# Performance work log

Hardware: AMD Instinct MI355X
Metric: run time of the kernel (lower is better)

Reference implementation:

```python
import jax, jax.numpy as jnp
import numpy as np

B, H, DH = 1, 16, 128
HID, MLP = 2048, 8192
LT, LI = 256, 2048
L = LT + LI


def _layernorm(x, eps=1e-6):
    mu = jnp.mean(x, axis=-1, keepdims=True)
    var = jnp.mean((x - mu) ** 2, axis=-1, keepdims=True)
    return (x - mu) * jax.lax.rsqrt(var + eps)


def _rmsnorm(x, scale, eps=1e-6):
    rr = jax.lax.rsqrt(jnp.mean(x * x, axis=-1, keepdims=True) + eps)
    return x * rr * scale


def _apply_rope(x, pe):
    # x: (B,H,L,D) -> (B,H,L,D/2,1,2); pe: (B,1,L,D/2,2,2)
    xs = x.reshape(*x.shape[:-1], -1, 1, 2)
    out = pe[..., 0] * xs[..., 0] + pe[..., 1] * xs[..., 1]  # (B,H,L,D/2,2)
    return out.reshape(x.shape)


def _qkv_split(x, w, b):
    Bv, Lv, _ = x.shape
    qkv = (x @ w + b).reshape(Bv, Lv, 3, H, DH).transpose(2, 0, 3, 1, 4)  # K B H L D
    return qkv[0], qkv[1], qkv[2]


def setup_inputs() -> dict:
    key = jax.random.key(0)
    ks = jax.random.split(key, 16)
    s = 0.02
    inp = {
        'img': jax.random.normal(ks[0], (B, LI, HID), jnp.float32),
        'txt': jax.random.normal(ks[1], (B, LT, HID), jnp.float32),
        'vec': jax.random.normal(ks[2], (B, HID), jnp.float32),
        'img_mod_w': s * jax.random.normal(ks[3], (HID, 6 * HID), jnp.float32),
        'img_mod_b': jnp.zeros((6 * HID,), jnp.float32),
        'txt_mod_w': s * jax.random.normal(ks[4], (HID, 6 * HID), jnp.float32),
        'txt_mod_b': jnp.zeros((6 * HID,), jnp.float32),
        'img_qkv_w': s * jax.random.normal(ks[5], (HID, 3 * HID), jnp.float32),
        'img_qkv_b': jnp.zeros((3 * HID,), jnp.float32),
        'img_q_scale': jnp.ones((DH,), jnp.float32),
        'img_k_scale': jnp.ones((DH,), jnp.float32),
        'txt_qkv_w': s * jax.random.normal(ks[6], (HID, 3 * HID), jnp.float32),
        'txt_qkv_b': jnp.zeros((3 * HID,), jnp.float32),
        'txt_q_scale': jnp.ones((DH,), jnp.float32),
        'txt_k_scale': jnp.ones((DH,), jnp.float32),
        'img_proj_w': s * jax.random.normal(ks[7], (HID, HID), jnp.float32),
        'img_proj_b': jnp.zeros((HID,), jnp.float32),
        'txt_proj_w': s * jax.random.normal(ks[8], (HID, HID), jnp.float32),
        'txt_proj_b': jnp.zeros((HID,), jnp.float32),
        'img_mlp_w1': s * jax.random.normal(ks[9], (HID, MLP), jnp.float32),
        'img_mlp_b1': jnp.zeros((MLP,), jnp.float32),
        'img_mlp_w2': s * jax.random.normal(ks[10], (MLP, HID), jnp.float32),
        'img_mlp_b2': jnp.zeros((HID,), jnp.float32),
        'txt_mlp_w1': s * jax.random.normal(ks[11], (HID, MLP), jnp.float32),
        'txt_mlp_b1': jnp.zeros((MLP,), jnp.float32),
        'txt_mlp_w2': s * jax.random.normal(ks[12], (MLP, HID), jnp.float32),
        'txt_mlp_b2': jnp.zeros((HID,), jnp.float32),
    }
    # Real RoPE rotation matrices [[cos,-sin],[sin,cos]]: (1,1,L,DH/2,2,2)
    pos = jnp.arange(L, dtype=jnp.float32)
    freqs = 1.0 / (10000.0 ** (jnp.arange(DH // 2, dtype=jnp.float32) / (DH // 2)))
    ang = pos[:, None] * freqs[None, :]
    c, sn = jnp.cos(ang), jnp.sin(ang)
    pe = jnp.stack([jnp.stack([c, -sn], -1), jnp.stack([sn, c], -1)], -2)  # (L,DH/2,2,2)
    inp['pe'] = pe[None, None]
    return inp


def reference(img, txt, vec, pe,
              img_mod_w, img_mod_b, txt_mod_w, txt_mod_b,
              img_qkv_w, img_qkv_b, img_q_scale, img_k_scale,
              txt_qkv_w, txt_qkv_b, txt_q_scale, txt_k_scale,
              img_proj_w, img_proj_b, txt_proj_w, txt_proj_b,
              img_mlp_w1, img_mlp_b1, img_mlp_w2, img_mlp_b2,
              txt_mlp_w1, txt_mlp_b1, txt_mlp_w2, txt_mlp_b2):
    # AdaLN modulation: SiLU(vec) @ W -> 6 chunks of (B,1,HID)
    im = jnp.split(jax.nn.silu(vec) @ img_mod_w + img_mod_b, 6, axis=-1)
    i_sh1, i_sc1, i_g1, i_sh2, i_sc2, i_g2 = [m[:, None, :] for m in im]
    tm = jnp.split(jax.nn.silu(vec) @ txt_mod_w + txt_mod_b, 6, axis=-1)
    t_sh1, t_sc1, t_g1, t_sh2, t_sc2, t_g2 = [m[:, None, :] for m in tm]

    img_mod = (1 + i_sc1) * _layernorm(img) + i_sh1
    iq, ik, iv = _qkv_split(img_mod, img_qkv_w, img_qkv_b)
    iq = _rmsnorm(iq, img_q_scale)
    ik = _rmsnorm(ik, img_k_scale)

    txt_mod = (1 + t_sc1) * _layernorm(txt) + t_sh1
    tq, tk, tv = _qkv_split(txt_mod, txt_qkv_w, txt_qkv_b)
    tq = _rmsnorm(tq, txt_q_scale)
    tk = _rmsnorm(tk, txt_k_scale)

    # concat text then image along sequence (B,H,L,D)
    q = jnp.concatenate([tq, iq], axis=2)
    k = jnp.concatenate([tk, ik], axis=2)
    v = jnp.concatenate([tv, iv], axis=2)
    q = _apply_rope(q, pe)
    k = _apply_rope(k, pe)

    scores = jnp.einsum('bhqd,bhkd->bhqk', q, k) / np.float32(np.sqrt(DH))
    a = jax.nn.softmax(scores, axis=-1)
    o = jnp.einsum('bhqk,bhkd->bhqd', a, v)
    attn = o.transpose(0, 2, 1, 3).reshape(o.shape[0], -1, H * DH)  # (B,L,HID)

    txt_a, img_a = attn[:, :LT], attn[:, LT:]

    img = img + i_g1 * (img_a @ img_proj_w + img_proj_b)
    h = (1 + i_sc2) * _layernorm(img) + i_sh2
    h = jax.nn.gelu(h @ img_mlp_w1 + img_mlp_b1, approximate=True)
    img = img + i_g2 * (h @ img_mlp_w2 + img_mlp_b2)

    txt = txt + t_g1 * (txt_a @ txt_proj_w + txt_proj_b)
    h = (1 + t_sc2) * _layernorm(txt) + t_sh2
    h = jax.nn.gelu(h @ txt_mlp_w1 + txt_mlp_b1, approximate=True)
    txt = txt + t_g2 * (h @ txt_mlp_w2 + txt_mlp_b2)

    return img, txt
```

## Files before the change

kernel.cpp:

```cpp
#include <hip/hip_runtime.h>

using u16 = unsigned short;
typedef __bf16 bf16x8 __attribute__((ext_vector_type(8)));
typedef float f32x4 __attribute__((ext_vector_type(4)));

__device__ inline u16 f2bf(float f){
  unsigned u = __float_as_uint(f);
  u += 0x7fff + ((u >> 16) & 1);
  return (u16)(u >> 16);
}
__device__ inline float bf2f(u16 u){ return __uint_as_float((unsigned)u << 16); }

__device__ inline float wredsum(float v){
  #pragma unroll
  for (int o = 32; o; o >>= 1) v += __shfl_xor(v, o, 64);
  return v;
}
__device__ inline float wredmax(float v){
  #pragma unroll
  for (int o = 32; o; o >>= 1) v = fmaxf(v, __shfl_xor(v, o, 64));
  return v;
}

__device__ inline void gld16(const u16* g, u16* lds){
  __builtin_amdgcn_global_load_lds(
      (const __attribute__((address_space(1))) unsigned int*)g,
      (__attribute__((address_space(3))) unsigned int*)lds, 16, 0, 0);
}

__global__ void mod_matvec_k(const float* __restrict__ vec,
    const float* __restrict__ wi, const float* __restrict__ bi,
    const float* __restrict__ wt, const float* __restrict__ bt,
    float* __restrict__ oi, float* __restrict__ ot)
{
  __shared__ float sv[2048];
  __shared__ float red[4][64];
  int tid = threadIdx.x;
  for (int i = tid; i < 2048; i += 256){ float v = vec[i]; sv[i] = v / (1.0f + __expf(-v)); }
  __syncthreads();
  int j0 = blockIdx.x * 64;
  bool ist = j0 >= 12288;
  const float* w = ist ? wt : wi;
  const float* b = ist ? bt : bi;
  float* o = ist ? ot : oi;
  int col = (ist ? j0 - 12288 : j0) + (tid & 63);
  int kq = tid >> 6;
  float acc = 0.f;
  const float* wp = w + col;
  for (int k = kq * 512; k < kq * 512 + 512; ++k) acc += sv[k] * wp[(long long)k * 12288];
  red[kq][tid & 63] = acc;
  __syncthreads();
  if (kq == 0){
    o[col] = red[0][tid] + red[1][tid] + red[2][tid] + red[3][tid] + b[col];
  }
}

struct TcArgs {
  const float* in[8];
  u16* out[8];
  int K[8];
  int N[8];
  int base[9];
};

__global__ void tcast8_k(TcArgs a)
{
  __shared__ float tile[32][33];
  int bid = blockIdx.x;
  int w = 0;
  #pragma unroll
  for (int i = 0; i < 8; ++i) if (bid >= a.base[i + 1]) w = i + 1;
  const float* in = a.in[w];
  u16* out = a.out[w];
// ... 44 lines not shown

__global__ void qkv_post_k(const float* __restrict__ qkv, int pos0,
    const float* __restrict__ qs, const float* __restrict__ ks,
    const float* __restrict__ pe,
    u16* __restrict__ Q, u16* __restrict__ Ko, u16* __restrict__ Vt)
{
  __shared__ u16 vs[128][72];
  int h = blockIdx.y;
  int t0 = blockIdx.x * 64;
  int tid = threadIdx.x, wave = tid >> 6, lane = tid & 63;
  for (int it = 0; it < 16; ++it){
    int tl = it * 4 + wave;
    int t = t0 + tl;
    const float* rp = qkv + (long long)t * 6144 + h * 128;
    float q0 = rp[lane],        q1 = rp[lane + 64];
    float k0 = rp[2048 + lane], k1 = rp[2048 + lane + 64];
    float v0 = rp[4096 + lane], v1 = rp[4096 + lane + 64];
    float qss = wredsum(q0 * q0 + q1 * q1);
    float kss = wredsum(k0 * k0 + k1 * k1);
    float rq = rsqrtf(qss * (1.0f / 128.0f) + 1e-6f) * 0.08838834764831845f;
    float rk = rsqrtf(kss * (1.0f / 128.0f) + 1e-6f);
    float qn0 = q0 * rq * qs[lane], qn1 = q1 * rq * qs[lane + 64];
    float kn0 = k0 * rk * ks[lane], kn1 = k1 * rk * ks[lane + 64];
    int pos = pos0 + t;
    const float* peb = pe + (long long)pos * 256;
    bool odd = lane & 1;
    float4 p0 = *(const float4*)&peb[(lane >> 1) * 4];
    float4 p1 = *(const float4*)&peb[128 + (lane >> 1) * 4];
    float c00 = odd ? p0.z : p0.x, c01 = odd ? p0.w : p0.y;
    float c10 = odd ? p1.z : p1.x, c11 = odd ? p1.w : p1.y;
    float qp0 = __shfl_xor(qn0, 1, 64), qp1 = __shfl_xor(qn1, 1, 64);
    float kp0 = __shfl_xor(kn0, 1, 64), kp1 = __shfl_xor(kn1, 1, 64);
    float qe0 = odd ? qp0 : qn0, qo0 = odd ? qn0 : qp0;
    float qe1 = odd ? qp1 : qn1, qo1 = odd ? qn1 : qp1;
    float ke0 = odd ? kp0 : kn0, ko0 = odd ? kn0 : kp0;
    float ke1 = odd ? kp1 : kn1, ko1 = odd ? kn1 : kp1;
    u16* Qr = Q  + ((long long)h * 2304 + pos) * 128;
    u16* Kr = Ko + ((long long)h * 2304 + pos) * 128;
    Qr[lane]      = f2bf(c00 * qe0 + c01 * qo0);
    Qr[lane + 64] = f2bf(c10 * qe1 + c11 * qo1);
    Kr[lane]      = f2bf(c00 * ke0 + c01 * ko0);
    Kr[lane + 64] = f2bf(c10 * ke1 + c11 * ko1);
    vs[lane][tl]      = f2bf(v0);
    vs[lane + 64][tl] = f2bf(v1);
  }
  __syncthreads();
  int dd = tid >> 1, co = (tid & 1) * 32;
  u16* vr = Vt + ((long long)h * 128 + dd) * 2304 + pos0 + t0 + co;
  #pragma unroll
  for (int u = 0; u < 8; ++u)
    *(ushort4*)(vr + u * 4) = *(const ushort4*)&vs[dd][co + u * 4];
}

__global__ void softmax16_k(u16* __restrict__ S)
{
  long long base = (long long)blockIdx.y * 2304 * 2304 + (long long)blockIdx.x * 2304;
  u16* row = S + base;
  int tid = threadIdx.x;
  float v[9]; float m = -3.0e38f;
  #pragma unroll
  for (int j = 0; j < 9; ++j){ v[j] = bf2f(row[tid + j * 256]); m = fmaxf(m, v[j]); }
  m = wredmax(m);
  __shared__ float red[4];
  int wave = tid >> 6, lane = tid & 63;
  if (lane == 0) red[wave] = m;
  __syncthreads();
  m = fmaxf(fmaxf(red[0], red[1]), fmaxf(red[2], red[3]));
  float s = 0.f;
  #pragma unroll
  for (int j = 0; j < 9; ++j){ v[j] = __expf(v[j] - m); s += v[j]; }
  s = wredsum(s);
  __syncthreads();
  if (lane == 0) red[wave] = s;
  __syncthreads();
  s = red[0] + red[1] + red[2] + red[3];
  float r = 1.0f / s;
  #pragma unroll
  for (int j = 0; j < 9; ++j) row[tid + j * 256] = f2bf(v[j] * r);
}

template<int MODE>
__global__ __launch_bounds__(512)
void gemm8_k(const u16* __restrict__ Ai, const u16* __restrict__ At, int lda,
             const u16* __restrict__ Bi, const u16* __restrict__ Bt, int ldb,
             const float* __restrict__ bias_i, const float* __restrict__ bias_t,
             const float* __restrict__ res_i,  const float* __restrict__ res_t,
             const float* __restrict__ gate_i, const float* __restrict__ gate_t,
             void* __restrict__ Ci, void* __restrict__ Ct, int ldc, int K)
{
  constexpr int BK = 64;
  constexpr int MR = 4, NR = 2;
  constexpr int AI = 2, BI = 2;

  __shared__ u16 As[2][128 * BK];
  __shared__ u16 Bs[2][128 * BK];

  const int tid  = threadIdx.x;
  const int lane = tid & 63;
  const int wave = tid >> 6;
  const int wm = wave >> 2;
  const int wn = wave & 3;

  const int gx = gridDim.x;
  const int nwg = gx * gridDim.y;
  const int n = blockIdx.x + gx * blockIdx.y;
  const int s_id = (n & 7) * (nwg >> 3) + (n >> 3);
  const int bx = s_id % gx;
  const int by = s_id / gx;

  const bool ist = bx >= 16;
  const int rb = ist ? bx - 16 : bx;
  const u16* Ab = (ist ? At : Ai) + (long long)rb * 128 * lda;
  const u16* Bb = (ist ? Bt : Bi) + (long long)by * 128 * ldb;
  const float* bias = ist ? bias_t : bias_i;
  const float* res  = ist ? res_t  : res_i;
  const float* gate = ist ? gate_t : gate_i;
  void* C = ist ? Ct : Ci;

  const int srow = wave * 8 + (lane >> 3);
  const int sgo  = ((lane & 7) ^ ((lane >> 3) & 7)) * 8;
  const u16* agp[AI]; const u16* bgp[BI];
  int alo[AI], blo[BI];
  #pragma unroll
  for (int i = 0; i < AI; ++i){
    agp[i] = Ab + (long long)(i * 64 + srow) * lda + sgo;
    alo[i] = (i * 64 + wave * 8) * BK;
  }
  #pragma unroll
  for (int i = 0; i < BI; ++i){
    bgp[i] = Bb + (long long)(i * 64 + srow) * ldb + sgo;
    blo[i] = (i * 64 + wave * 8) * BK;
  }

  const int arow0 = wm * 64;
  const int frow  = lane & 15;
  const int fx    = lane & 7;
  const int j0    = lane >> 4;

  f32x4 acc[MR][NR] = {};

  #pragma unroll
  for (int i = 0; i < AI; ++i) gld16(agp[i], &As[0][alo[i]]);
  #pragma unroll
  for (int i = 0; i < BI; ++i) gld16(bgp[i], &Bs[0][blo[i]]);
  __builtin_amdgcn_sched_barrier(0);

  const int nt = K / BK;
  for (int t = 0; t < nt; ++t){
    if (t + 1 < nt){
      int k0 = (t + 1) * BK;
      int nb = (t + 1) & 1;
      #pragma unroll
      for (int i = 0; i < AI; ++i) gld16(agp[i] + k0, &As[nb][alo[i]]);
      #pragma unroll
      for (int i = 0; i < BI; ++i) gld16(bgp[i] + k0, &Bs[nb][blo[i]]);
      __builtin_amdgcn_sched_barrier(0);
      asm volatile("s_waitcnt vmcnt(4)" ::: "memory");
    } else {
      asm volatile("s_waitcnt vmcnt(0)" ::: "memory");
    }
    __builtin_amdgcn_sched_barrier(0);
    __builtin_amdgcn_s_barrier();
    __builtin_amdgcn_sched_barrier(0);

    const u16* as = As[t & 1];
    const u16* bs = Bs[t & 1];
    #pragma unroll
    for (int s = 0; s < 2; ++s){
      const int oct = (s * 4 + j0) ^ fx;
      bf16x8 bfr[NR];
      #pragma unroll
      for (int nn = 0; nn < NR; ++nn)
        bfr[nn] = *(const bf16x8*)&bs[(wn * 32 + nn * 16 + frow) * BK + oct * 8];
      __builtin_amdgcn_s_setprio(1);
      #pragma unroll
      for (int m = 0; m < MR; ++m){
        bf16x8 af = *(const bf16x8*)&as[(arow0 + m * 16 + frow) * BK + oct * 8];
        #pragma unroll
        for (int nn = 0; nn < NR; ++nn)
          acc[m][nn] = __builtin_amdgcn_mfma_f32_16x16x32_bf16(af, bfr[nn], acc[m][nn], 0, 0, 0);
      }
      __builtin_amdgcn_s_setprio(0);
    }
    __builtin_amdgcn_sched_barrier(0);
    __builtin_amdgcn_s_barrier();
    __builtin_amdgcn_sched_barrier(0);
  }

  const int lr = (lane >> 4) * 4;
  const int lc = lane & 15;
  const long long rowb = (long long)rb * 128 + arow0;
  const long long colb = (long long)by * 128 + wn * 32;
  #pragma unroll
  for (int mi = 0; mi < MR; ++mi){
    #pragma unroll
    for (int ni = 0; ni < NR; ++ni){
      long long col = colb + ni * 16 + lc;
      float bv = bias ? bias[col] : 0.0f;
      #pragma unroll
      for (int j = 0; j < 4; ++j){
        long long row = rowb + mi * 16 + lr + j;
        float v = acc[mi][ni][j] + bv;
        long long ci = row * (long long)ldc + col;
        if constexpr (MODE == 0) ((float*)C)[ci] = v;
        else if constexpr (MODE == 2) ((float*)C)[ci] = res[ci] + gate[col] * v;
        else {
          float z2 = 1.5957691216057308f * (v + 0.044715f * v * v * v);
          ((u16*)C)[ci] = f2bf(v / (1.0f + __expf(-z2)));
        }
      }
    }
  }
}

template<int BM, int BN, int MODE>
__global__ __launch_bounds__(256)
void gemm_k(const u16* __restrict__ A, int lda, long long abstr,
            const u16* __restrict__ B, int ldb, long long bbstr,
            void* __restrict__ C, int ldc, long long cbstr,
            int K)
{
  constexpr int BK  = 32;
  constexpr int WGM = BM / 64;
  constexpr int WGN = 4 / WGM;
  constexpr int WTN = BN / WGN;
  constexpr int NFR = WTN / 16;
  constexpr int CA  = BM / 64;
  constexpr int CB  = BN / 64;

  __shared__ u16 As[2][BM * BK];
  __shared__ u16 Bs[2][BN * BK];
  const int tid  = threadIdx.x;
  const int lane = tid & 63;
  const int wave = tid >> 6;
  const int wr = (wave / WGN) * 64;
  const int wc = (wave % WGN) * WTN;

  const u16* Ab = A + (long long)blockIdx.z * abstr + (long long)blockIdx.x * BM * lda;
  const u16* Bb = B + (long long)blockIdx.z * bbstr + (long long)blockIdx.y * BN * ldb;

  const int srow = lane >> 2;
  const int scol = (lane & 3) * 8;
  const u16* agp[CA]; int aro[CA];
  const u16* bgp[CB]; int bro[CB];
  #pragma unroll
  for (int c = 0; c < CA; ++c){
    int r0 = (c * 4 + wave) * 16;
    agp[c] = Ab + (long long)(r0 + srow) * lda + scol;
    aro[c] = r0 * BK;
  }
  #pragma unroll
  for (int c = 0; c < CB; ++c){
    int r0 = (c * 4 + wave) * 16;
    bgp[c] = Bb + (long long)(r0 + srow) * ldb + scol;
    bro[c] = r0 * BK;
  }

  #pragma unroll
  for (int c = 0; c < CA; ++c) gld16(agp[c], &As[0][aro[c]]);
  #pragma unroll
  for (int c = 0; c < CB; ++c) gld16(bgp[c], &Bs[0][bro[c]]);
  __syncthreads();

  f32x4 acc[4][NFR] = {};
  const int nt = K / BK;
  int cur = 0;
  for (int t = 0; t < nt; ++t){
    int nxt = cur ^ 1;
    if (t + 1 < nt){
      int ko = (t + 1) * BK;
      #pragma unroll
      for (int c = 0; c < CA; ++c) gld16(agp[c] + ko, &As[nxt][aro[c]]);
      #pragma unroll
      for (int c = 0; c < CB; ++c) gld16(bgp[c] + ko, &Bs[nxt][bro[c]]);
    }
    bf16x8 af[4], bfr[NFR];
    #pragma unroll
    for (int i = 0; i < 4; ++i)
      af[i] = *(const bf16x8*)&As[cur][(wr + i * 16 + (lane & 15)) * BK + (lane >> 4) * 8];
    #pragma unroll
    for (int i = 0; i < NFR; ++i)
      bfr[i] = *(const bf16x8*)&Bs[cur][(wc + i * 16 + (lane & 15)) * BK + (lane >> 4) * 8];
    #pragma unroll
    for (int mi = 0; mi < 4; ++mi)
      #pragma unroll
      for (int ni = 0; ni < NFR; ++ni)
        acc[mi][ni] = __builtin_amdgcn_mfma_f32_16x16x32_bf16(af[mi], bfr[ni], acc[mi][ni], 0, 0, 0);
    __syncthreads();
    cur = nxt;
  }

  const int lr = (lane >> 4) * 4;
  const int lc = lane & 15;
  const long long rowb = (long long)blockIdx.x * BM + wr;
  const long long colb = (long long)blockIdx.y * BN + wc;
  const long long cb = (long long)blockIdx.z * cbstr;
  #pragma unroll
  for (int mi = 0; mi < 4; ++mi){
    #pragma unroll
    for (int ni = 0; ni < NFR; ++ni){
      long long col = colb + ni * 16 + lc;
      #pragma unroll
      for (int j = 0; j < 4; ++j){
        long long row = rowb + mi * 16 + lr + j;
        float v = acc[mi][ni][j];
        long long ci = cb + row * ldc + col;
        if constexpr (MODE == 0) ((float*)C)[ci] = v;
        else ((u16*)C)[ci] = f2bf(v);
      }
    }
  }
}

extern "C" void kernel_launch(void* const* d_in, const int* in_sizes, int n_in,
                              void* d_out, int out_size, void* d_ws, size_t ws_size,
                              hipStream_t stream)
{
  const float* img        = (const float*)d_in[0];
  const float* txt        = (const float*)d_in[1];
  const float* vec        = (const float*)d_in[2];
  const float* img_mod_w  = (const float*)d_in[3];
  const float* img_mod_b  = (const float*)d_in[4];
  const float* txt_mod_w  = (const float*)d_in[5];
  const float* txt_mod_b  = (const float*)d_in[6];
  const float* img_qkv_w  = (const float*)d_in[7];
  const float* img_qkv_b  = (const float*)d_in[8];
  const float* img_q_s    = (const float*)d_in[9];
  const float* img_k_s    = (const float*)d_in[10];
  const float* txt_qkv_w  = (const float*)d_in[11];
  const float* txt_qkv_b  = (const float*)d_in[12];
  const float* txt_q_s    = (const float*)d_in[13];
  const float* txt_k_s    = (const float*)d_in[14];
  const float* img_proj_w = (const float*)d_in[15];
  const float* img_proj_b = (const float*)d_in[16];
  const float* txt_proj_w = (const float*)d_in[17];
  const float* txt_proj_b = (const float*)d_in[18];
  const float* img_mlp_w1 = (const float*)d_in[19];
  const float* img_mlp_b1 = (const float*)d_in[20];
  const float* img_mlp_w2 = (const float*)d_in[21];
  const float* img_mlp_b2 = (const float*)d_in[22];
  const float* txt_mlp_w1 = (const float*)d_in[23];
  const float* txt_mlp_b1 = (const float*)d_in[24];
  const float* txt_mlp_w2 = (const float*)d_in[25];
  const float* txt_mlp_b2 = (const float*)d_in[26];
  const float* pe         = (const float*)d_in[27];

  char* ws = (char*)d_ws;
  size_t off = 0;
  auto alloc = [&](size_t b){ void* p = ws + off; off = (off + b + 255) & ~(size_t)255; return p; };

  u16* wq_i = (u16*)alloc(6144ll * 2048 * 2);
  u16* wq_t = (u16*)alloc(6144ll * 2048 * 2);
  u16* wp_i = (u16*)alloc(2048ll * 2048 * 2);
  u16* wp_t = (u16*)alloc(2048ll * 2048 * 2);
  u16* w1_i = (u16*)alloc(8192ll * 2048 * 2);
  u16* w1_t = (u16*)alloc(8192ll * 2048 * 2);
  u16* w2_i = (u16*)alloc(2048ll * 8192 * 2);
  u16* w2_t = (u16*)alloc(2048ll * 8192 * 2);
  float* mod_i = (float*)alloc(12288 * 4);
  float* mod_t = (float*)alloc(12288 * 4);
  u16* Qb   = (u16*)alloc(16ll * 2304 * 128 * 2);
  u16* Kb   = (u16*)alloc(16ll * 2304 * 128 * 2);
  u16* Vt   = (u16*)alloc(16ll * 2304 * 128 * 2);
  u16* attn = (u16*)alloc(2304ll * 2048 * 2);
  char* big = (char*)alloc(4ll * 2304 * 2304 * 4);

  size_t s16_bytes = 16ll * 2304 * 2304 * 2;
  size_t off_before_s16 = off;
  u16* S16 = (u16*)alloc(s16_bytes);
  const bool merged_attn = (off <= ws_size);
  if (!merged_attn) off = off_before_s16;

  u16*   xin_i = (u16*)big;
  u16*   xin_t = (u16*)(big + 8388608);
  float* qkv_i = (float*)(big + 9437184);
  float* qkv_t = (float*)(big + 59768832);
  u16*   S4   = (u16*)big;
  float* y1_i  = (float*)big;
  float* y1_t  = (float*)(big + 16777216);
  u16*   ln2_i = (u16*)(big + 18874368);
  u16*   ln2_t = (u16*)(big + 27262976);
  u16*   h_i   = (u16*)(big + 28311552);
  u16*   h_t   = (u16*)(big + 61865984);

  mod_matvec_k<<<384, 256, 0, stream>>>(vec, img_mod_w, img_mod_b, txt_mod_w, txt_mod_b, mod_i, mod_t);

  {
    TcArgs a;
    const float* ins[8] = {img_qkv_w, txt_qkv_w, img_proj_w, txt_proj_w,
                           img_mlp_w1, txt_mlp_w1, img_mlp_w2, txt_mlp_w2};
    u16* outs[8] = {wq_i, wq_t, wp_i, wp_t, w1_i, w1_t, w2_i, w2_t};
    int Ks[8] = {2048, 2048, 2048, 2048, 2048, 2048, 8192, 8192};
    int Ns[8] = {6144, 6144, 2048, 2048, 8192, 8192, 2048, 2048};
    int b = 0;
    for (int i = 0; i < 8; ++i){
      a.in[i] = ins[i]; a.out[i] = outs[i]; a.K[i] = Ks[i]; a.N[i] = Ns[i];
      a.base[i] = b;
      b += (Ks[i] >> 5) * (Ns[i] >> 5);
    }
    a.base[8] = b;
    tcast8_k<<<b, 256, 0, stream>>>(a);
  }

  ln_mod_k<<<2048, 256, 0, stream>>>(img, mod_i, mod_i + 2048, xin_i);
  ln_mod_k<<<256,  256, 0, stream>>>(txt, mod_t, mod_t + 2048, xin_t);

  gemm8_k<0><<<dim3(18, 48), 512, 0, stream>>>(xin_i, xin_t, 2048, wq_i, wq_t, 2048,
      img_qkv_b, txt_qkv_b, nullptr, nullptr, nullptr, nullptr, qkv_i, qkv_t, 6144, 2048);

  qkv_post_k<<<dim3(32, 16), 256, 0, stream>>>(qkv_i, 256, img_q_s, img_k_s, pe, Qb, Kb, Vt);
  qkv_post_k<<<dim3(4, 16),  256, 0, stream>>>(qkv_t, 0,   txt_q_s, txt_k_s, pe, Qb, Kb, Vt);

  if (merged_attn){
    gemm_k<128,128,1><<<dim3(18, 18, 16), 256, 0, stream>>>(Qb, 128, 2304ll * 128, Kb, 128, 2304ll * 128,
        S16, 2304, 2304ll * 2304, 128);
    softmax16_k<<<dim3(2304, 16), 256, 0, stream>>>(S16);
    gemm_k<128,64,1><<<dim3(18, 2, 16), 256, 0, stream>>>(S16, 2304, 2304ll * 2304, Vt, 2304, 128ll * 2304,
        attn, 2048, 128, 2304);
  } else {
    for (int g = 0; g < 4; ++g){
      const u16* Qg = Qb + (long long)g * 4 * 2304 * 128;
      const u16* Kg = Kb + (long long)g * 4 * 2304 * 128;
      const u16* Vg = Vt + (long long)g * 4 * 128 * 2304;
      gemm_k<128,128,1><<<dim3(18, 18, 4), 256, 0, stream>>>(Qg, 128, 2304ll * 128, Kg, 128, 2304ll * 128,
          S4, 2304, 2304ll * 2304, 128);
      softmax16_k<<<dim3(2304, 4), 256, 0, stream>>>(S4);
      gemm_k<128,64,1><<<dim3(18, 2, 4), 256, 0, stream>>>(S4, 2304, 2304ll * 2304, Vg, 2304, 128ll * 2304,
          attn + g * 4 * 128, 2048, 128, 2304);
    }
  }

  gemm8_k<2><<<dim3(18, 16), 512, 0, stream>>>(attn + 256 * 2048, attn, 2048, wp_i, wp_t, 2048,
      img_proj_b, txt_proj_b, img, txt, mod_i + 4096, mod_t + 4096, y1_i, y1_t, 2048, 2048);

  ln_mod_k<<<2048, 256, 0, stream>>>(y1_i, mod_i + 6144, mod_i + 8192, ln2_i);
  ln_mod_k<<<256,  256, 0, stream>>>(y1_t, mod_t + 6144, mod_t + 8192, ln2_t);

  gemm8_k<3><<<dim3(18, 64), 512, 0, stream>>>(ln2_i, ln2_t, 2048, w1_i, w1_t, 2048,
      img_mlp_b1, txt_mlp_b1, nullptr, nullptr, nullptr, nullptr, h_i, h_t, 8192, 2048);

  float* out_img = (float*)d_out;
  float* out_txt = out_img + 2048ll * 2048;
  gemm8_k<2><<<dim3(18, 16), 512, 0, stream>>>(h_i, h_t, 8192, w2_i, w2_t, 8192,
      img_mlp_b2, txt_mlp_b2, y1_i, y1_t, mod_i + 10240, mod_t + 10240, out_img, out_txt, 2048, 8192);
}
```

Before: 883.7 us.

## Replace 128x128 fused GEMM with 256-row tiles and quadrant-split pipelined staging

The dual-stream GEMM moves from 128x128 tiles to 256xBN tiles (BN=256 for the QKV and MLP-up GEMMs, 128 for the projection GEMMs). Each K step is split into four quadrant sub-steps, and half-tile loads for the next and next-next K slices are issued between them, giving deeper prefetch. The larger tiles raise operand reuse per LDS byte and cut redundant global loads. In exchange, LDS use goes up, the grid is much smaller (fewer workgroups than CUs for some GEMMs), the text rows now take a 256-row tile holding only 256 real rows, the XCD swizzle is dropped, and there are more barriers per K step.

Measured after the change: 1.051 ms. 18.9% more time.

```diff
diff --git a/kernel.cpp b/kernel.cpp
--- a/kernel.cpp
+++ b/kernel.cpp
@@ -196,39 +196,37 @@
   for (int j = 0; j < 9; ++j) row[tid + j * 256] = f2bf(v[j] * r);
 }
 
-template<int MODE>
+template<int BN, int MODE>
 __global__ __launch_bounds__(512)
-void gemm8_k(const u16* __restrict__ Ai, const u16* __restrict__ At, int lda,
+void gemm9_k(const u16* __restrict__ Ai, const u16* __restrict__ At, int lda,
              const u16* __restrict__ Bi, const u16* __restrict__ Bt, int ldb,
              const float* __restrict__ bias_i, const float* __restrict__ bias_t,
              const float* __restrict__ res_i,  const float* __restrict__ res_t,
              const float* __restrict__ gate_i, const float* __restrict__ gate_t,
              void* __restrict__ Ci, void* __restrict__ Ct, int ldc, int K)
 {
-  constexpr int BK = 64;
-  constexpr int MR = 4, NR = 2;
-  constexpr int AI = 2, BI = 2;
-
-  __shared__ u16 As[2][128 * BK];
-  __shared__ u16 Bs[2][128 * BK];
+  constexpr int BK  = 64;
+  constexpr int BNH = BN / 2;
+  constexpr int WM  = (BN == 256) ? 2 : 4;
+  constexpr int WN  = 8 / WM;
+  constexpr int MRH = 128 / (WM * 16);
+  constexpr int NRH = BNH / (WN * 16);
+  constexpr int BL  = (BNH == 128) ? 2 : 1;
+
+  __shared__ u16 Ah[2][2][128 * BK];
+  __shared__ u16 Bh[2][2][BNH * BK];
 
   const int tid  = threadIdx.x;
   const int lane = tid & 63;
   const int wave = tid >> 6;
-  const int wm = wave >> 2;
-  const int wn = wave & 3;
-
-  const int gx = gridDim.x;
-  const int nwg = gx * gridDim.y;
-  const int n = blockIdx.x + gx * blockIdx.y;
-  const int s_id = (n & 7) * (nwg >> 3) + (n >> 3);
-  const int bx = s_id % gx;
-  const int by = s_id / gx;
-
-  const bool ist = bx >= 16;
-  const int rb = ist ? bx - 16 : bx;
-  const u16* Ab = (ist ? At : Ai) + (long long)rb * 128 * lda;
-  const u16* Bb = (ist ? Bt : Bi) + (long long)by * 128 * ldb;
+  const int wm   = wave % WM;
+  const int wn   = wave / WM;
+
+  const int bx = blockIdx.x;
+  const int by = blockIdx.y;
+  const bool ist = (bx == 8);
+  const u16* Ab = ist ? At : (Ai + (long long)bx * 256 * lda);
+  const u16* Bb = (ist ? Bt : Bi) + (long long)by * BN * ldb;
   const float* bias = ist ? bias_t : bias_i;
   const float* res  = ist ? res_t  : res_i;
   const float* gate = ist ? gate_t : gate_i;
@@ -236,88 +234,96 @@
 
   const int srow = wave * 8 + (lane >> 3);
   const int sgo  = ((lane & 7) ^ ((lane >> 3) & 7)) * 8;
-  const u16* agp[AI]; const u16* bgp[BI];
-  int alo[AI], blo[BI];
-  #pragma unroll
-  for (int i = 0; i < AI; ++i){
-    agp[i] = Ab + (long long)(i * 64 + srow) * lda + sgo;
-    alo[i] = (i * 64 + wave * 8) * BK;
-  }
-  #pragma unroll
-  for (int i = 0; i < BI; ++i){
-    bgp[i] = Bb + (long long)(i * 64 + srow) * ldb + sgo;
-    blo[i] = (i * 64 + wave * 8) * BK;
-  }
-
-  const int arow0 = wm * 64;
-  const int frow  = lane & 15;
-  const int fx    = lane & 7;
-  const int j0    = lane >> 4;
-
-  f32x4 acc[MR][NR] = {};
-
-  #pragma unroll
-  for (int i = 0; i < AI; ++i) gld16(agp[i], &As[0][alo[i]]);
-  #pragma unroll
-  for (int i = 0; i < BI; ++i) gld16(bgp[i], &Bs[0][blo[i]]);
+
+  auto stageA = [&](int h, int b, int kk){
+    #pragma unroll
+    for (int j = 0; j < 2; ++j)
+      gld16(Ab + (long long)(h * 128 + j * 64 + srow) * lda + kk + sgo,
+            &Ah[b][h][(j * 64 + wave * 8) * BK]);
+  };
+  auto stageB = [&](int h, int b, int kk){
+    #pragma unroll
+    for (int j = 0; j < BL; ++j)
+      gld16(Bb + (long long)(h * BNH + j * 64 + srow) * ldb + kk + sgo,
+            &Bh[b][h][(j * 64 + wave * 8) * BK]);
+  };
+
+  const int frow = lane & 15;
+  const int fx   = lane & 7;
+  const int j0   = lane >> 4;
+
+  f32x4 acc[2 * MRH][2 * NRH] = {};
+
+  const int nt = K / BK;
+  stageA(0, 0, 0); stageB(0, 0, 0); stageA(1, 0, 0); stageB(1, 0, 0);
+  stageA(0, 1, BK); stageB(0, 1, BK);
   __builtin_amdgcn_sched_barrier(0);
 
-  const int nt = K / BK;
   for (int t = 0; t < nt; ++t){
-    if (t + 1 < nt){
-      int k0 = (t + 1) * BK;
-      int nb = (t + 1) & 1;
-      #pragma unroll
-      for (int i = 0; i < AI; ++i) gld16(agp[i] + k0, &As[nb][alo[i]]);
-      #pragma unroll
-      for (int i = 0; i < BI; ++i) gld16(bgp[i] + k0, &Bs[nb][blo[i]]);
+    const int b = t & 1;
+    #pragma unroll
+    for (int q = 0; q < 4; ++q){
+      if      (q == 0){ if (t + 1 < nt) stageA(1, (t + 1) & 1, (t + 1) * BK); }
+      else if (q == 1){ if (t + 1 < nt) stageB(1, (t + 1) & 1, (t + 1) * BK); }
+      else if (q == 2){ if (t + 2 < nt) stageA(0, b, (t + 2) * BK); }
+      else            { if (t + 2 < nt) stageB(0, b, (t + 2) * BK); }
       __builtin_amdgcn_sched_barrier(0);
-      asm volatile("s_waitcnt vmcnt(4)" ::: "memory");
-    } else {
-      asm volatile("s_waitcnt vmcnt(0)" ::: "memory");
+      if (q == 0){
+        if (t == nt - 1)              asm volatile("s_waitcnt vmcnt(0)" ::: "memory");
+        else if constexpr (BN == 256) asm volatile("s_waitcnt vmcnt(6)" ::: "memory");
+        else                          asm volatile("s_waitcnt vmcnt(5)" ::: "memory");
+        __builtin_amdgcn_sched_barrier(0);
+      }
+      __builtin_amdgcn_s_barrier();
+      __builtin_amdgcn_sched_barrier(0);
+
+      const int mh = q >> 1, nh = q & 1;
+      const u16* as = Ah[b][mh];
+      const u16* bs = Bh[b][nh];
+      bf16x8 af[2][MRH], bfr[2][NRH];
+      #pragma unroll
+      for (int s = 0; s < 2; ++s){
+        const int oct = ((s * 4 + j0) ^ fx) * 8;
+        #pragma unroll
+        for (int i = 0; i < MRH; ++i)
+          af[s][i] = *(const bf16x8*)&as[(wm * (128 / WM) + i * 16 + frow) * BK + oct];
+        #pragma unroll
+        for (int i = 0; i < NRH; ++i)
+          bfr[s][i] = *(const bf16x8*)&bs[(wn * 32 + i * 16 + frow) * BK + oct];
+      }
+      asm volatile("s_waitcnt lgkmcnt(0)" ::: "memory");
+      __builtin_amdgcn_sched_barrier(0);
+      __builtin_amdgcn_s_setprio(1);
+      #pragma unroll
+      for (int s = 0; s < 2; ++s)
+        #pragma unroll
+        for (int i = 0; i < MRH; ++i)
+          #pragma unroll
+          for (int k2 = 0; k2 < NRH; ++k2)
+            acc[mh * MRH + i][nh * NRH + k2] = __builtin_amdgcn_mfma_f32_16x16x32_bf16(
+                af[s][i], bfr[s][k2], acc[mh * MRH + i][nh * NRH + k2], 0, 0, 0);
+      __builtin_amdgcn_s_setprio(0);
+      __builtin_amdgcn_sched_barrier(0);
+      __builtin_amdgcn_s_barrier();
+      __builtin_amdgcn_sched_barrier(0);
     }
-    __builtin_amdgcn_sched_barrier(0);
-    __builtin_amdgcn_s_barrier();
-    __builtin_amdgcn_sched_barrier(0);
-
-    const u16* as = As[t & 1];
-    const u16* bs = Bs[t & 1];
-    #pragma unroll
-    for (int s = 0; s < 2; ++s){
-      const int oct = (s * 4 + j0) ^ fx;
-      bf16x8 bfr[NR];
-      #pragma unroll
-      for (int nn = 0; nn < NR; ++nn)
-        bfr[nn] = *(const bf16x8*)&bs[(wn * 32 + nn * 16 + frow) * BK + oct * 8];
-      __builtin_amdgcn_s_setprio(1);
-      #pragma unroll
-      for (int m = 0; m < MR; ++m){
-        bf16x8 af = *(const bf16x8*)&as[(arow0 + m * 16 + frow) * BK + oct * 8];
-        #pragma unroll
-        for (int nn = 0; nn < NR; ++nn)
-          acc[m][nn] = __builtin_amdgcn_mfma_f32_16x16x32_bf16(af, bfr[nn], acc[m][nn], 0, 0, 0);
-      }
-      __builtin_amdgcn_s_setprio(0);
-    }
-    __builtin_amdgcn_sched_barrier(0);
-    __builtin_amdgcn_s_barrier();
-    __builtin_amdgcn_sched_barrier(0);
   }
 
   const int lr = (lane >> 4) * 4;
   const int lc = lane & 15;
-  const long long rowb = (long long)rb * 128 + arow0;
-  const long long colb = (long long)by * 128 + wn * 32;
-  #pragma unroll
-  for (int mi = 0; mi < MR; ++mi){
-    #pragma unroll
-    for (int ni = 0; ni < NR; ++ni){
-      long long col = colb + ni * 16 + lc;
+  const long long rowbase = ist ? 0 : (long long)bx * 256;
+  #pragma unroll
+  for (int m = 0; m < 2 * MRH; ++m){
+    const int mh = m / MRH, im = m % MRH;
+    #pragma unroll
+    for (int n = 0; n < 2 * NRH; ++n){
+      const int nh = n / NRH, in_ = n % NRH;
+      long long col = (long long)by * BN + nh * BNH + wn * 32 + in_ * 16 + lc;
       float bv = bias ? bias[col] : 0.0f;
       #pragma unroll
-      for (int j = 0; j < 4; ++j){
-        long long row = rowb + mi * 16 + lr + j;
-        float v = acc[mi][ni][j] + bv;
+      for (int jj = 0; jj < 4; ++jj){
+        long long row = rowbase + mh * 128 + wm * (128 / WM) + im * 16 + lr + jj;
+        float v = acc[m][n][jj] + bv;
         long long ci = row * (long long)ldc + col;
         if constexpr (MODE == 0) ((float*)C)[ci] = v;
         else if constexpr (MODE == 2) ((float*)C)[ci] = res[ci] + gate[col] * v;
@@ -522,7 +528,7 @@
   ln_mod_k<<<2048, 256, 0, stream>>>(img, mod_i, mod_i + 2048, xin_i);
   ln_mod_k<<<256,  256, 0, stream>>>(txt, mod_t, mod_t + 2048, xin_t);
 
-  gemm8_k<0><<<dim3(18, 48), 512, 0, stream>>>(xin_i, xin_t, 2048, wq_i, wq_t, 2048,
+  gemm9_k<256,0><<<dim3(9, 24), 512, 0, stream>>>(xin_i, xin_t, 2048, wq_i, wq_t, 2048,
       img_qkv_b, txt_qkv_b, nullptr, nullptr, nullptr, nullptr, qkv_i, qkv_t, 6144, 2048);
 
   qkv_post_k<<<dim3(32, 16), 256, 0, stream>>>(qkv_i, 256, img_q_s, img_k_s, pe, Qb, Kb, Vt);
@@ -547,17 +553,17 @@
     }
   }
 
-  gemm8_k<2><<<dim3(18, 16), 512, 0, stream>>>(attn + 256 * 2048, attn, 2048, wp_i, wp_t, 2048,
+  gemm9_k<128,2><<<dim3(9, 16), 512, 0, stream>>>(attn + 256 * 2048, attn, 2048, wp_i, wp_t, 2048,
       img_proj_b, txt_proj_b, img, txt, mod_i + 4096, mod_t + 4096, y1_i, y1_t, 2048, 2048);
 
   ln_mod_k<<<2048, 256, 0, stream>>>(y1_i, mod_i + 6144, mod_i + 8192, ln2_i);
   ln_mod_k<<<256,  256, 0, stream>>>(y1_t, mod_t + 6144, mod_t + 8192, ln2_t);
 
-  gemm8_k<3><<<dim3(18, 64), 512, 0, stream>>>(ln2_i, ln2_t, 2048, w1_i, w1_t, 2048,
+  gemm9_k<256,3><<<dim3(9, 32), 512, 0, stream>>>(ln2_i, ln2_t, 2048, w1_i, w1_t, 2048,
       img_mlp_b1, txt_mlp_b1, nullptr, nullptr, nullptr, nullptr, h_i, h_t, 8192, 2048);
 
   float* out_img = (float*)d_out;
   float* out_txt = out_img + 2048ll * 2048;
-  gemm8_k<2><<<dim3(18, 16), 512, 0, stream>>>(h_i, h_t, 8192, w2_i, w2_t, 8192,
+  gemm9_k<128,2><<<dim3(9, 16), 512, 0, stream>>>(h_i, h_t, 8192, w2_i, w2_t, 8192,
       img_mlp_b2, txt_mlp_b2, y1_i, y1_t, mod_i + 10240, mod_t + 10240, out_img, out_txt, 2048, 8192);
 }
```

## Split-K the projection and MLP-down GEMMs with a separate combine epilogue

Applied to the files above, without the earlier changes.

The two N=2048 GEMMs (attention projection and MLP second layer) launched only 288 workgroups. They now use split-K with two K halves along blockIdx.z, which doubles the grid to better fill the CUs. Each half writes fp32 partials to a new workspace buffer. A new combine kernel adds the partials, bias, gated residual and writes the outputs. The cost is an extra fp32 partial write and read of about 38 MB per GEMM and two extra launches.

After: 893.6 us. No clear change (+1.1%).

```diff
diff --git a/kernel.cpp b/kernel.cpp
--- a/kernel.cpp
+++ b/kernel.cpp
@@ -196,6 +196,40 @@
   for (int j = 0; j < 9; ++j) row[tid + j * 256] = f2bf(v[j] * r);
 }
 
+__global__ void combine_k(const float* __restrict__ p, long long czoff,
+    const float* __restrict__ bias_i, const float* __restrict__ bias_t,
+    const float* __restrict__ res_i,  const float* __restrict__ res_t,
+    const float* __restrict__ gate_i, const float* __restrict__ gate_t,
+    float* __restrict__ outi, float* __restrict__ outt)
+{
+  int row = blockIdx.x;
+  bool ist = row >= 2048;
+  int r = ist ? row - 2048 : row;
+  const float* bias = ist ? bias_t : bias_i;
+  const float* res  = ist ? res_t  : res_i;
+  const float* gate = ist ? gate_t : gate_i;
+  float* out = ist ? outt : outi;
+  const float* p0 = p + (long long)row * 2048;
+  const float* p1 = p0 + czoff;
+  long long base = (long long)r * 2048;
+  int j0 = threadIdx.x * 4;
+  #pragma unroll
+  for (int it = 0; it < 2; ++it){
+    int j = j0 + it * 1024;
+    float4 a = *(const float4*)&p0[j];
+    float4 b = *(const float4*)&p1[j];
+    float4 bi4 = *(const float4*)&bias[j];
+    float4 g = *(const float4*)&gate[j];
+    float4 rr = *(const float4*)&res[base + j];
+    float4 o;
+    o.x = rr.x + g.x * (a.x + b.x + bi4.x);
+    o.y = rr.y + g.y * (a.y + b.y + bi4.y);
+    o.z = rr.z + g.z * (a.z + b.z + bi4.z);
+    o.w = rr.w + g.w * (a.w + b.w + bi4.w);
+    *(float4*)&out[base + j] = o;
+  }
+}
+
 template<int MODE>
 __global__ __launch_bounds__(512)
 void gemm8_k(const u16* __restrict__ Ai, const u16* __restrict__ At, int lda,
@@ -203,7 +237,8 @@
              const float* __restrict__ bias_i, const float* __restrict__ bias_t,
              const float* __restrict__ res_i,  const float* __restrict__ res_t,
              const float* __restrict__ gate_i, const float* __restrict__ gate_t,
-             void* __restrict__ Ci, void* __restrict__ Ct, int ldc, int K)
+             void* __restrict__ Ci, void* __restrict__ Ct, int ldc, int K,
+             int kz, long long czoff)
 {
   constexpr int BK = 64;
   constexpr int MR = 4, NR = 2;
@@ -224,11 +259,12 @@
   const int s_id = (n & 7) * (nwg >> 3) + (n >> 3);
   const int bx = s_id % gx;
   const int by = s_id / gx;
+  const int bz = blockIdx.z;
 
   const bool ist = bx >= 16;
   const int rb = ist ? bx - 16 : bx;
-  const u16* Ab = (ist ? At : Ai) + (long long)rb * 128 * lda;
-  const u16* Bb = (ist ? Bt : Bi) + (long long)by * 128 * ldb;
+  const u16* Ab = (ist ? At : Ai) + (long long)rb * 128 * lda + (long long)bz * kz;
+  const u16* Bb = (ist ? Bt : Bi) + (long long)by * 128 * ldb + (long long)bz * kz;
   const float* bias = ist ? bias_t : bias_i;
   const float* res  = ist ? res_t  : res_i;
   const float* gate = ist ? gate_t : gate_i;
@@ -308,6 +344,7 @@
   const int lc = lane & 15;
   const long long rowb = (long long)rb * 128 + arow0;
   const long long colb = (long long)by * 128 + wn * 32;
+  const long long cz = (long long)bz * czoff;
   #pragma unroll
   for (int mi = 0; mi < MR; ++mi){
     #pragma unroll
@@ -319,7 +356,7 @@
         long long row = rowb + mi * 16 + lr + j;
         float v = acc[mi][ni][j] + bv;
         long long ci = row * (long long)ldc + col;
-        if constexpr (MODE == 0) ((float*)C)[ci] = v;
+        if constexpr (MODE == 0) ((float*)C)[ci + cz] = v;
         else if constexpr (MODE == 2) ((float*)C)[ci] = res[ci] + gate[col] * v;
         else {
           float z2 = 1.5957691216057308f * (v + 0.044715f * v * v * v);
@@ -480,6 +517,7 @@
   u16* Kb   = (u16*)alloc(16ll * 2304 * 128 * 2);
   u16* Vt   = (u16*)alloc(16ll * 2304 * 128 * 2);
   u16* attn = (u16*)alloc(2304ll * 2048 * 2);
+  float* part = (float*)alloc(2ll * 2304 * 2048 * 4);
   char* big = (char*)alloc(4ll * 2304 * 2304 * 4);
 
   size_t s16_bytes = 16ll * 2304 * 2304 * 2;
@@ -499,6 +537,10 @@
   u16*   ln2_t = (u16*)(big + 27262976);
   u16*   h_i   = (u16*)(big + 28311552);
   u16*   h_t   = (u16*)(big + 61865984);
+
+  const long long CZ = 2304ll * 2048;
+  float* pimg = part;
+  float* ptxt = part + 2048ll * 2048;
 
   mod_matvec_k<<<384, 256, 0, stream>>>(vec, img_mod_w, img_mod_b, txt_mod_w, txt_mod_b, mod_i, mod_t);
 
@@ -523,7 +565,7 @@
   ln_mod_k<<<256,  256, 0, stream>>>(txt, mod_t, mod_t + 2048, xin_t);
 
   gemm8_k<0><<<dim3(18, 48), 512, 0, stream>>>(xin_i, xin_t, 2048, wq_i, wq_t, 2048,
-      img_qkv_b, txt_qkv_b, nullptr, nullptr, nullptr, nullptr, qkv_i, qkv_t, 6144, 2048);
+      img_qkv_b, txt_qkv_b, nullptr, nullptr, nullptr, nullptr, qkv_i, qkv_t, 6144, 2048, 0, 0);
 
   qkv_post_k<<<dim3(32, 16), 256, 0, stream>>>(qkv_i, 256, img_q_s, img_k_s, pe, Qb, Kb, Vt);
   qkv_post_k<<<dim3(4, 16),  256, 0, stream>>>(qkv_t, 0,   txt_q_s, txt_k_s, pe, Qb, Kb, Vt);
@@ -547,17 +589,21 @@
     }
   }
 
-  gemm8_k<2><<<dim3(18, 16), 512, 0, stream>>>(attn + 256 * 2048, attn, 2048, wp_i, wp_t, 2048,
-      img_proj_b, txt_proj_b, img, txt, mod_i + 4096, mod_t + 4096, y1_i, y1_t, 2048, 2048);
+  gemm8_k<0><<<dim3(18, 16, 2), 512, 0, stream>>>(attn + 256 * 2048, attn, 2048, wp_i, wp_t, 2048,
+      nullptr, nullptr, nullptr, nullptr, nullptr, nullptr, pimg, ptxt, 2048, 1024, 1024, CZ);
+  combine_k<<<2304, 256, 0, stream>>>(part, CZ, img_proj_b, txt_proj_b, img, txt,
+      mod_i + 4096, mod_t + 4096, y1_i, y1_t);
 
   ln_mod_k<<<2048, 256, 0, stream>>>(y1_i, mod_i + 6144, mod_i + 8192, ln2_i);
   ln_mod_k<<<256,  256, 0, stream>>>(y1_t, mod_t + 6144, mod_t + 8192, ln2_t);
 
   gemm8_k<3><<<dim3(18, 64), 512, 0, stream>>>(ln2_i, ln2_t, 2048, w1_i, w1_t, 2048,
-      img_mlp_b1, txt_mlp_b1, nullptr, nullptr, nullptr, nullptr, h_i, h_t, 8192, 2048);
+      img_mlp_b1, txt_mlp_b1, nullptr, nullptr, nullptr, nullptr, h_i, h_t, 8192, 2048, 0, 0);
 
   float* out_img = (float*)d_out;
   float* out_txt = out_img + 2048ll * 2048;
-  gemm8_k<2><<<dim3(18, 16), 512, 0, stream>>>(h_i, h_t, 8192, w2_i, w2_t, 8192,
-      img_mlp_b2, txt_mlp_b2, y1_i, y1_t, mod_i + 10240, mod_t + 10240, out_img, out_txt, 2048, 8192);
-}
+  gemm8_k<0><<<dim3(18, 16, 2), 512, 0, stream>>>(h_i, h_t, 8192, w2_i, w2_t, 8192,
+      nullptr, nullptr, nullptr, nullptr, nullptr, nullptr, pimg, ptxt, 2048, 4096, 4096, CZ);
+  combine_k<<<2304, 256, 0, stream>>>(part, CZ, img_mlp_b2, txt_mlp_b2, y1_i, y1_t,
+      mod_i + 10240, mod_t + 10240, out_img, out_txt);
+}
```

## Replace materialized attention scores with fused flash-attention kernel

Applied to the files above, without the earlier changes.

Replaces the three-kernel attention path (QK^T GEMM writing a full 16x2304x2304 bf16 score matrix, a row softmax, then a PV GEMM) with a single flash-attention kernel. The new kernel uses online softmax, swizzled LDS tiles of K and double-buffered V, and MFMA for both products. This removes the large HBM round-trips for the score matrix and two kernel launches. In exchange the grid has only 288 blocks of 512 threads with heavy LDS use, so occupancy and parallelism across CUs are limited.

New measurement: 863.2 us. 1.02x faster.

```diff
diff --git a/kernel.cpp b/kernel.cpp
--- a/kernel.cpp
+++ b/kernel.cpp
@@ -9,16 +9,10 @@
   u += 0x7fff + ((u >> 16) & 1);
   return (u16)(u >> 16);
 }
-__device__ inline float bf2f(u16 u){ return __uint_as_float((unsigned)u << 16); }
 
 __device__ inline float wredsum(float v){
   #pragma unroll
   for (int o = 32; o; o >>= 1) v += __shfl_xor(v, o, 64);
-  return v;
-}
-__device__ inline float wredmax(float v){
-  #pragma unroll
-  for (int o = 32; o; o >>= 1) v = fmaxf(v, __shfl_xor(v, o, 64));
   return v;
 }
 
@@ -169,31 +163,137 @@
     *(ushort4*)(vr + u * 4) = *(const ushort4*)&vs[dd][co + u * 4];
 }
 
-__global__ void softmax16_k(u16* __restrict__ S)
-{
-  long long base = (long long)blockIdx.y * 2304 * 2304 + (long long)blockIdx.x * 2304;
-  u16* row = S + base;
-  int tid = threadIdx.x;
-  float v[9]; float m = -3.0e38f;
-  #pragma unroll
-  for (int j = 0; j < 9; ++j){ v[j] = bf2f(row[tid + j * 256]); m = fmaxf(m, v[j]); }
-  m = wredmax(m);
-  __shared__ float red[4];
-  int wave = tid >> 6, lane = tid & 63;
-  if (lane == 0) red[wave] = m;
-  __syncthreads();
-  m = fmaxf(fmaxf(red[0], red[1]), fmaxf(red[2], red[3]));
-  float s = 0.f;
-  #pragma unroll
-  for (int j = 0; j < 9; ++j){ v[j] = __expf(v[j] - m); s += v[j]; }
-  s = wredsum(s);
-  __syncthreads();
-  if (lane == 0) red[wave] = s;
-  __syncthreads();
-  s = red[0] + red[1] + red[2] + red[3];
-  float r = 1.0f / s;
-  #pragma unroll
-  for (int j = 0; j < 9; ++j) row[tid + j * 256] = f2bf(v[j] * r);
+__global__ __launch_bounds__(512)
+void fattn_k(const u16* __restrict__ Qb, const u16* __restrict__ Kb,
+             const u16* __restrict__ Vt, u16* __restrict__ attn)
+{
+  __shared__ u16 Pl[128 * 128];
+  __shared__ u16 Kl[128 * 128];
+  __shared__ u16 Vl[2][128 * 128];
+
+  const int tid  = threadIdx.x;
+  const int lane = tid & 63;
+  const int wave = tid >> 6;
+  const int h  = blockIdx.y;
+  const int q0 = blockIdx.x * 128;
+
+  const u16* Qg = Qb + ((long long)h * 2304 + q0) * 128;
+  const u16* Kg = Kb + (long long)h * 2304 * 128;
+  const u16* Vg = Vt + (long long)h * 128 * 2304;
+
+  const int s_r   = wave * 4 + (lane >> 4);
+  const int s_oct = lane & 15;
+  auto stage = [&](const u16* g, int ldg, u16* lds){
+    #pragma unroll
+    for (int i = 0; i < 4; ++i){
+      int row = i * 32 + s_r;
+      gld16(g + (long long)row * ldg + ((s_oct ^ (row & 7)) * 8),
+            lds + (i * 32 + wave * 4) * 128);
+    }
+  };
+
+  stage(Qg, 128, Pl);
+  stage(Kg, 128, Kl);
+  stage(Vg, 2304, Vl[0]);
+  __syncthreads();
+
+  const int frow = lane & 15;
+  const int j0   = lane >> 4;
+  const int qrow = wave * 16 + frow;
+  bf16x8 aq[4];
+  #pragma unroll
+  for (int s = 0; s < 4; ++s)
+    aq[s] = *(const bf16x8*)&Pl[qrow * 128 + (((s * 4 + j0) ^ (qrow & 7)) * 8)];
+  __syncthreads();
+
+  float mrun[4], lrun[4];
+  #pragma unroll
+  for (int j = 0; j < 4; ++j){ mrun[j] = -3.0e38f; lrun[j] = 0.f; }
+  f32x4 oacc[8] = {};
+
+  for (int t = 0; t < 18; ++t){
+    asm volatile("s_waitcnt vmcnt(0)" ::: "memory");
+    __builtin_amdgcn_sched_barrier(0);
+    __builtin_amdgcn_s_barrier();
+    __builtin_amdgcn_sched_barrier(0);
+
+    f32x4 sacc[8] = {};
+    #pragma unroll
+    for (int s = 0; s < 4; ++s){
+      #pragma unroll
+      for (int n = 0; n < 8; ++n){
+        int kr = n * 16 + frow;
+        bf16x8 bk = *(const bf16x8*)&Kl[kr * 128 + (((s * 4 + j0) ^ (kr & 7)) * 8)];
+        sacc[n] = __builtin_amdgcn_mfma_f32_16x16x32_bf16(aq[s], bk, sacc[n], 0, 0, 0);
+      }
+    }
+    __builtin_amdgcn_sched_barrier(0);
+    __builtin_amdgcn_s_barrier();
+    __builtin_amdgcn_sched_barrier(0);
+    if (t + 1 < 18){
+      stage(Kg + (long long)(t + 1) * 128 * 128, 128, Kl);
+      stage(Vg + (t + 1) * 128, 2304, Vl[(t + 1) & 1]);
+    }
+    __builtin_amdgcn_sched_barrier(0);
+
+    float mnew[4], scl[4];
+    #pragma unroll
+    for (int j = 0; j < 4; ++j){
+      float v = sacc[0][j];
+      #pragma unroll
+      for (int n = 1; n < 8; ++n) v = fmaxf(v, sacc[n][j]);
+      #pragma unroll
+      for (int o = 8; o; o >>= 1) v = fmaxf(v, __shfl_xor(v, o, 64));
+      mnew[j] = fmaxf(mrun[j], v);
+      scl[j] = __expf(mrun[j] - mnew[j]);
+      mrun[j] = mnew[j];
+    }
+    #pragma unroll
+    for (int j = 0; j < 4; ++j){
+      const int row = wave * 16 + j0 * 4 + j;
+      float rsum = 0.f;
+      #pragma unroll
+      for (int n = 0; n < 8; ++n){
+        float p = __expf(sacc[n][j] - mnew[j]);
+        rsum += p;
+        int col = n * 16 + frow;
+        Pl[row * 128 + (((col >> 3) ^ (row & 7)) << 3) + (col & 7)] = f2bf(p);
+      }
+      #pragma unroll
+      for (int o = 8; o; o >>= 1) rsum += __shfl_xor(rsum, o, 64);
+      lrun[j] = lrun[j] * scl[j] + rsum;
+      #pragma unroll
+      for (int n = 0; n < 8; ++n) oacc[n][j] *= scl[j];
+    }
+    asm volatile("s_waitcnt lgkmcnt(0)" ::: "memory");
+    __builtin_amdgcn_sched_barrier(0);
+
+    const u16* vl = Vl[t & 1];
+    #pragma unroll
+    for (int s = 0; s < 4; ++s){
+      bf16x8 ap = *(const bf16x8*)&Pl[qrow * 128 + (((s * 4 + j0) ^ (qrow & 7)) * 8)];
+      #pragma unroll
+      for (int n = 0; n < 8; ++n){
+        int dr = n * 16 + frow;
+        bf16x8 bv = *(const bf16x8*)&vl[dr * 128 + (((s * 4 + j0) ^ (dr & 7)) * 8)];
+        oacc[n] = __builtin_amdgcn_mfma_f32_16x16x32_bf16(ap, bv, oacc[n], 0, 0, 0);
+      }
+    }
+    __builtin_amdgcn_sched_barrier(0);
+  }
+
+  float inv[4];
+  #pragma unroll
+  for (int j = 0; j < 4; ++j) inv[j] = 1.0f / lrun[j];
+  #pragma unroll
+  for (int n = 0; n < 8; ++n){
+    int d = n * 16 + frow;
+    #pragma unroll
+    for (int j = 0; j < 4; ++j){
+      int row = wave * 16 + j0 * 4 + j;
+      attn[(long long)(q0 + row) * 2048 + h * 128 + d] = f2bf(oacc[n][j] * inv[j]);
+    }
+  }
 }
 
 template<int MODE>
@@ -325,105 +425,6 @@
           float z2 = 1.5957691216057308f * (v + 0.044715f * v * v * v);
           ((u16*)C)[ci] = f2bf(v / (1.0f + __expf(-z2)));
         }
-      }
-    }
-  }
-}
-
-template<int BM, int BN, int MODE>
-__global__ __launch_bounds__(256)
-void gemm_k(const u16* __restrict__ A, int lda, long long abstr,
-            const u16* __restrict__ B, int ldb, long long bbstr,
-            void* __restrict__ C, int ldc, long long cbstr,
-            int K)
-{
-  constexpr int BK  = 32;
-  constexpr int WGM = BM / 64;
-  constexpr int WGN = 4 / WGM;
-  constexpr int WTN = BN / WGN;
-  constexpr int NFR = WTN / 16;
-  constexpr int CA  = BM / 64;
-  constexpr int CB  = BN / 64;
-
-  __shared__ u16 As[2][BM * BK];
-  __shared__ u16 Bs[2][BN * BK];
-  const int tid  = threadIdx.x;
-  const int lane = tid & 63;
-  const int wave = tid >> 6;
-  const int wr = (wave / WGN) * 64;
-  const int wc = (wave % WGN) * WTN;
-
-  const u16* Ab = A + (long long)blockIdx.z * abstr + (long long)blockIdx.x * BM * lda;
-  const u16* Bb = B + (long long)blockIdx.z * bbstr + (long long)blockIdx.y * BN * ldb;
-
-  const int srow = lane >> 2;
-  const int scol = (lane & 3) * 8;
-  const u16* agp[CA]; int aro[CA];
-  const u16* bgp[CB]; int bro[CB];
-  #pragma unroll
-  for (int c = 0; c < CA; ++c){
-    int r0 = (c * 4 + wave) * 16;
-    agp[c] = Ab + (long long)(r0 + srow) * lda + scol;
-    aro[c] = r0 * BK;
-  }
-  #pragma unroll
-  for (int c = 0; c < CB; ++c){
-    int r0 = (c * 4 + wave) * 16;
-    bgp[c] = Bb + (long long)(r0 + srow) * ldb + scol;
-    bro[c] = r0 * BK;
-  }
-
-  #pragma unroll
-  for (int c = 0; c < CA; ++c) gld16(agp[c], &As[0][aro[c]]);
-  #pragma unroll
-  for (int c = 0; c < CB; ++c) gld16(bgp[c], &Bs[0][bro[c]]);
-  __syncthreads();
-
-  f32x4 acc[4][NFR] = {};
-  const int nt = K / BK;
-  int cur = 0;
-  for (int t = 0; t < nt; ++t){
-    int nxt = cur ^ 1;
-    if (t + 1 < nt){
-      int ko = (t + 1) * BK;
-      #pragma unroll
-      for (int c = 0; c < CA; ++c) gld16(agp[c] + ko, &As[nxt][aro[c]]);
-      #pragma unroll
-      for (int c = 0; c < CB; ++c) gld16(bgp[c] + ko, &Bs[nxt][bro[c]]);
-    }
-    bf16x8 af[4], bfr[NFR];
-    #pragma unroll
-    for (int i = 0; i < 4; ++i)
-      af[i] = *(const bf16x8*)&As[cur][(wr + i * 16 + (lane & 15)) * BK + (lane >> 4) * 8];
-    #pragma unroll
-    for (int i = 0; i < NFR; ++i)
-      bfr[i] = *(const bf16x8*)&Bs[cur][(wc + i * 16 + (lane & 15)) * BK + (lane >> 4) * 8];
-    #pragma unroll
-    for (int mi = 0; mi < 4; ++mi)
-      #pragma unroll
-      for (int ni = 0; ni < NFR; ++ni)
-        acc[mi][ni] = __builtin_amdgcn_mfma_f32_16x16x32_bf16(af[mi], bfr[ni], acc[mi][ni], 0, 0, 0);
-    __syncthreads();
-    cur = nxt;
-  }
-
-  const int lr = (lane >> 4) * 4;
-  const int lc = lane & 15;
-  const long long rowb = (long long)blockIdx.x * BM + wr;
-  const long long colb = (long long)blockIdx.y * BN + wc;
-  const long long cb = (long long)blockIdx.z * cbstr;
-  #pragma unroll
-  for (int mi = 0; mi < 4; ++mi){
-    #pragma unroll
-    for (int ni = 0; ni < NFR; ++ni){
-      long long col = colb + ni * 16 + lc;
-      #pragma unroll
-      for (int j = 0; j < 4; ++j){
-        long long row = rowb + mi * 16 + lr + j;
-        float v = acc[mi][ni][j];
-        long long ci = cb + row * ldc + col;
-        if constexpr (MODE == 0) ((float*)C)[ci] = v;
-        else ((u16*)C)[ci] = f2bf(v);
       }
     }
   }
@@ -482,17 +483,10 @@
   u16* attn = (u16*)alloc(2304ll * 2048 * 2);
   char* big = (char*)alloc(4ll * 2304 * 2304 * 4);
 
-  size_t s16_bytes = 16ll * 2304 * 2304 * 2;
-  size_t off_before_s16 = off;
-  u16* S16 = (u16*)alloc(s16_bytes);
-  const bool merged_attn = (off <= ws_size);
-  if (!merged_attn) off = off_before_s16;
-
   u16*   xin_i = (u16*)big;
   u16*   xin_t = (u16*)(big + 8388608);
   float* qkv_i = (float*)(big + 9437184);
   float* qkv_t = (float*)(big + 59768832);
-  u16*   S4   = (u16*)big;
   float* y1_i  = (float*)big;
   float* y1_t  = (float*)(big + 16777216);
   u16*   ln2_i = (u16*)(big + 18874368);
@@ -528,24 +522,7 @@
   qkv_post_k<<<dim3(32, 16), 256, 0, stream>>>(qkv_i, 256, img_q_s, img_k_s, pe, Qb, Kb, Vt);
   qkv_post_k<<<dim3(4, 16),  256, 0, stream>>>(qkv_t, 0,   txt_q_s, txt_k_s, pe, Qb, Kb, Vt);
 
-  if (merged_attn){
-    gemm_k<128,128,1><<<dim3(18, 18, 16), 256, 0, stream>>>(Qb, 128, 2304ll * 128, Kb, 128, 2304ll * 128,
-        S16, 2304, 2304ll * 2304, 128);
-    softmax16_k<<<dim3(2304, 16), 256, 0, stream>>>(S16);
-    gemm_k<128,64,1><<<dim3(18, 2, 16), 256, 0, stream>>>(S16, 2304, 2304ll * 2304, Vt, 2304, 128ll * 2304,
-        attn, 2048, 128, 2304);
-  } else {
-    for (int g = 0; g < 4; ++g){
-      const u16* Qg = Qb + (long long)g * 4 * 2304 * 128;
-      const u16* Kg = Kb + (long long)g * 4 * 2304 * 128;
-      const u16* Vg = Vt + (long long)g * 4 * 128 * 2304;
-      gemm_k<128,128,1><<<dim3(18, 18, 4), 256, 0, stream>>>(Qg, 128, 2304ll * 128, Kg, 128, 2304ll * 128,
-          S4, 2304, 2304ll * 2304, 128);
-      softmax16_k<<<dim3(2304, 4), 256, 0, stream>>>(S4);
-      gemm_k<128,64,1><<<dim3(18, 2, 4), 256, 0, stream>>>(S4, 2304, 2304ll * 2304, Vg, 2304, 128ll * 2304,
-          attn + g * 4 * 128, 2048, 128, 2304);
-    }
-  }
+  fattn_k<<<dim3(18, 16), 512, 0, stream>>>(Qb, Kb, Vt, attn);
 
   gemm8_k<2><<<dim3(18, 16), 512, 0, stream>>>(attn + 256 * 2048, attn, 2048, wp_i, wp_t, 2048,
       img_proj_b, txt_proj_b, img, txt, mod_i + 4096, mod_t + 4096, y1_i, y1_t, 2048, 2048);
```
